# Optimization experiments

Measured on AMD Instinct MI355X. Metric: run time of the kernel, lower is better.

## Reference

```python
import jax, jax.numpy as jnp
import numpy as np

B, T, D = 4, 1024, 1024
H, KVH = 16, 4
HD = D // H
DFF = 4096
WINDOW = 256
EPS = 1e-5


def _layernorm(x, g, b):
    mu = jnp.mean(x, axis=-1, keepdims=True)
    var = jnp.mean(jnp.square(x - mu), axis=-1, keepdims=True)
    return (x - mu) * jax.lax.rsqrt(var + EPS) * g + b


def _rope(x):
    # x: (B, H, T, HD); non-interleaved halves, matching _apply_rope
    half = HD // 2
    theta = 1.0 / (10000.0 ** (jnp.arange(half, dtype=jnp.float32) / half))
    pos = jnp.arange(x.shape[2], dtype=jnp.float32)
    freqs = jnp.outer(pos, theta)            # (T, half)
    cos_f, sin_f = jnp.cos(freqs), jnp.sin(freqs)
    x1, x2 = x[..., :half], x[..., half:]
    return jnp.concatenate([x1 * cos_f - x2 * sin_f, x2 * cos_f + x1 * sin_f], axis=-1)


def setup_inputs() -> dict:
    key = jax.random.key(0)
    ks = jax.random.split(key, 16)
    s = 0.02
    d = {
        "x": jax.random.normal(ks[0], (B, T, D), dtype=jnp.float32),
        "Wq": jax.random.normal(ks[1], (D, H * HD), dtype=jnp.float32) * s,
        "bq": jnp.zeros((H * HD,), jnp.float32),
        "Wk": jax.random.normal(ks[2], (D, KVH * HD), dtype=jnp.float32) * s,
        "bk": jnp.zeros((KVH * HD,), jnp.float32),
        "Wv": jax.random.normal(ks[3], (D, KVH * HD), dtype=jnp.float32) * s,
        "bv": jnp.zeros((KVH * HD,), jnp.float32),
        "Wo": jax.random.normal(ks[4], (D, D), dtype=jnp.float32) * s,
        "bo": jnp.zeros((D,), jnp.float32),
        "g1": jnp.ones((D,), jnp.float32),
        "b1": jnp.zeros((D,), jnp.float32),
        "Wf1": jax.random.normal(ks[5], (D, DFF), dtype=jnp.float32) * s,
        "bf1": jnp.zeros((DFF,), jnp.float32),
        "Wf2": jax.random.normal(ks[6], (DFF, D), dtype=jnp.float32) * s,
        "bf2": jnp.zeros((D,), jnp.float32),
        "g2": jnp.ones((D,), jnp.float32),
        "b2": jnp.zeros((D,), jnp.float32),
    }
    return d


def reference(x, Wq, bq, Wk, bk, Wv, bv, Wo, bo, g1, b1, Wf1, bf1, Wf2, bf2, g2, b2):
    Bt, Tt, _ = x.shape
    h = _layernorm(x, g1, b1)
    q = (h @ Wq + bq).reshape(Bt, Tt, H, HD).transpose(0, 2, 1, 3)      # (B,H,T,HD)
    k = (h @ Wk + bk).reshape(Bt, Tt, KVH, HD).transpose(0, 2, 1, 3)    # (B,KVH,T,HD)
    v = (h @ Wv + bv).reshape(Bt, Tt, KVH, HD).transpose(0, 2, 1, 3)
    # GQA: repeat_interleave kv heads to nhead
    group = H // KVH
    k = jnp.repeat(k, group, axis=1)
    v = jnp.repeat(v, group, axis=1)
    q, k = _rope(q), _rope(k)
    scores = jnp.einsum("bhqd,bhkd->bhqk", q, k) / jnp.sqrt(jnp.float32(HD))
    # causal sliding-window mask: attend iff 0 <= (row-col) < WINDOW
    row = jnp.arange(Tt)[:, None]
    col = jnp.arange(Tt)[None, :]
    valid = (col <= row) & (row - col < WINDOW)
    scores = jnp.where(valid, scores, jnp.float32(-1e9))
    attn = jax.nn.softmax(scores, axis=-1)
    out = jnp.einsum("bhqk,bhkd->bhqd", attn, v)
    out = out.transpose(0, 2, 1, 3).reshape(Bt, Tt, D)
    x = x + (out @ Wo + bo)
    h2 = _layernorm(x, g2, b2)
    ff = jax.nn.gelu(h2 @ Wf1 + bf1, approximate=False) @ Wf2 + bf2
    return x + ff
```

## Files before the change

### kernel.cpp

```cpp
#include <hip/hip_runtime.h>
#include <hip/hip_bf16.h>
#include <math.h>

#define TT 1024
#define DD 1024
#define HH 16
#define KVHN 4
#define HDW 64
#define DFFN 4096
#define WIN 256

typedef __attribute__((ext_vector_type(4))) float f32x4;
typedef __attribute__((ext_vector_type(8))) __bf16 bf16x8;

typedef const __attribute__((address_space(1))) void gas_t;
typedef __attribute__((address_space(3))) void las_t;

__device__ inline unsigned short f2bf(float f){
  union { float f; unsigned u; } x; x.f = f;
  unsigned r = x.u + 0x7fffu + ((x.u >> 16) & 1u);
  return (unsigned short)(r >> 16);
}
__device__ inline float bf2f(unsigned short b){
  union { unsigned u; float f; } x; x.u = ((unsigned)b) << 16; return x.f;
}
__device__ inline f32x4 MFMA(bf16x8 a, bf16x8 b, f32x4 c){
  return __builtin_amdgcn_mfma_f32_16x16x32_bf16(a, b, c, 0, 0, 0);
}

__global__ void zero_k(float* out, int n){
  for (int i = blockIdx.x * blockDim.x + threadIdx.x; i < n; i += gridDim.x * blockDim.x)
    out[i] = 0.f;
}

__global__ __launch_bounds__(256) void wtrans_k(const float* __restrict__ W,
                                                unsigned short* __restrict__ Wt,
                                                int K, int N){
  __shared__ float t[32][33];
  int n0 = blockIdx.x * 32, k0 = blockIdx.y * 32;
  int tx = threadIdx.x & 31, ty = threadIdx.x >> 5;
#pragma unroll
  for (int i = 0; i < 4; i++){
    int kk = ty * 4 + i;
    t[kk][tx] = W[(size_t)(k0 + kk) * N + n0 + tx];
  }
  __syncthreads();
#pragma unroll
  for (int i = 0; i < 4; i++){
    int nn = ty * 4 + i;
    Wt[(size_t)(n0 + nn) * K + k0 + tx] = f2bf(t[tx][nn]);
  }
}

__global__ void packb_k(const float* bq, const float* bk, const float* bv, float* o){
  int i = blockIdx.x * 256 + threadIdx.x;
  if (i < 1536)
    o[i] = (i < 1024) ? bq[i] : ((i < 1280) ? bk[i - 1024] : bv[i - 1280]);
}

__global__ void finit_k(const float* __restrict__ x2, const float* __restrict__ bf2,
                        float* __restrict__ out){
  for (int i = blockIdx.x * blockDim.x + threadIdx.x; i < 4096 * 1024; i += gridDim.x * blockDim.x)
    out[i] = x2[i] + bf2[i & 1023];
}

__global__ __launch_bounds__(256) void ln_k(const float* __restrict__ x,
                                            const float* __restrict__ g,
                                            const float* __restrict__ b,
                                            unsigned short* __restrict__ out){
  __shared__ float red[4];
  int row = blockIdx.x, tid = threadIdx.x;
  const float* xr = x + (size_t)row * DD;
  float4 v = *(const float4*)(xr + tid * 4);
  float s = v.x + v.y + v.z + v.w;
#pragma unroll
  for (int off = 32; off; off >>= 1) s += __shfl_xor(s, off);
  if ((tid & 63) == 0) red[tid >> 6] = s;
  __syncthreads();
  float mu = (red[0] + red[1] + red[2] + red[3]) * (1.f / DD);
  __syncthreads();
  float dx = v.x - mu, dy = v.y - mu, dz = v.z - mu, dw = v.w - mu;
  float sq = dx*dx + dy*dy + dz*dz + dw*dw;
#pragma unroll
  for (int off = 32; off; off >>= 1) sq += __shfl_xor(sq, off);
  if ((tid & 63) == 0) red[tid >> 6] = sq;
  __syncthreads();
  float var = (red[0] + red[1] + red[2] + red[3]) * (1.f / DD);
  float inv = rsqrtf(var + 1e-5f);
  float4 gv = *(const float4*)(g + tid * 4);
  float4 bv = *(const float4*)(b + tid * 4);
  unsigned short* orow = out + (size_t)row * DD + tid * 4;
  orow[0] = f2bf(dx * inv * gv.x + bv.x);
  orow[1] = f2bf(dy * inv * gv.y + bv.y);
  orow[2] = f2bf(dz * inv * gv.z + bv.z);
  orow[3] = f2bf(dw * inv * gv.w + bv.w);
}

template<int EPI>
__global__ __launch_bounds__(512, 2) void gemm256_k(const unsigned short* __restrict__ A,
                                                    const unsigned short* __restrict__ Bt,
                                                    const float* __restrict__ bias,
                                                    void* __restrict__ Cout,
                                                    int M, int N, int Klen, int lda, int ldb){
  __shared__ unsigned short As2[2][16384];
  __shared__ unsigned short Bs2[2][16384];
  int tid = threadIdx.x;
  int row0 = blockIdx.x * 256, col0 = blockIdx.y * 256;
  int wid = tid >> 6, lane = tid & 63;
  int wr = wid >> 2, wc = wid & 3;
  int lr = lane & 15, lg = lane >> 4;
  int srow8 = tid >> 3;
  int schunk = (tid & 7) ^ (srow8 & 7);
  int xr8 = (lr & 7) << 3;
  f32x4 acc[8][4] = {};

  auto stageA = [&](int slot, int half, int ktn){
    const unsigned short* s0 = A + (size_t)(row0 + half*128 + srow8) * lda + ktn*64 + schunk*8;
    __builtin_amdgcn_global_load_lds((gas_t*)s0, (las_t*)&As2[slot][half*8192 + wid*512], 16, 0, 0);
    __builtin_amdgcn_global_load_lds((gas_t*)(s0 + (size_t)64*lda), (las_t*)&As2[slot][half*8192 + 4096 + wid*512], 16, 0, 0);
  };
  auto stageB = [&](int slot, int half, int ktn){
    const unsigned short* s0 = Bt + (size_t)(col0 + half*128 + srow8) * ldb + ktn*64 + schunk*8;
    __builtin_amdgcn_global_load_lds((gas_t*)s0, (las_t*)&Bs2[slot][half*8192 + wid*512], 16, 0, 0);
    __builtin_amdgcn_global_load_lds((gas_t*)(s0 + (size_t)64*ldb), (las_t*)&Bs2[slot][half*8192 + 4096 + wid*512], 16, 0, 0);
  };

  int NT = Klen >> 6;
  stageA(0, 0, 0); stageA(0, 1, 0); stageB(0, 0, 0); stageB(0, 1, 0);
  __syncthreads();

  for (int kt = 0; kt < NT; kt++){
    int s = kt & 1, ns = s ^ 1;
    bool pre = (kt + 1 < NT);
    const unsigned short* Ac = &As2[s][wr * 8192];
    const unsigned short* Bc = &Bs2[s][(wc >> 1) * 8192 + (wc & 1) * 4096];
    bf16x8 af[4][2], bf0[2][2], bf1[2][2];

#pragma unroll
    for (int mf = 0; mf < 4; mf++)
#pragma unroll
      for (int ks = 0; ks < 2; ks++)
        af[mf][ks] = *(const bf16x8*)&Ac[(mf*16 + lr)*64 + ((ks*32 + lg*8) ^ xr8)];
#pragma unroll
    for (int nf = 0; nf < 2; nf++)
#pragma unroll
      for (int ks = 0; ks < 2; ks++)
        bf0[nf][ks] = *(const bf16x8*)&Bc[(nf*16 + lr)*64 + ((ks*32 + lg*8) ^ xr8)];
    if (pre) stageA(ns, 0, kt + 1);
    __builtin_amdgcn_s_barrier();
    __builtin_amdgcn_s_setprio(1);
#pragma unroll
    for (int mf = 0; mf < 4; mf++)
#pragma unroll
      for (int nf = 0; nf < 2; nf++)
#pragma unroll
        for (int ks = 0; ks < 2; ks++)
          acc[mf][nf] = MFMA(af[mf][ks], bf0[nf][ks], acc[mf][nf]);
    __builtin_amdgcn_s_setprio(0);
    __builtin_amdgcn_s_barrier();

#pragma unroll
    for (int nf = 0; nf < 2; nf++)
#pragma unroll
      for (int ks = 0; ks < 2; ks++)
        bf1[nf][ks] = *(const bf16x8*)&Bc[((nf+2)*16 + lr)*64 + ((ks*32 + lg*8) ^ xr8)];
    if (pre) stageA(ns, 1, kt + 1);
    __builtin_amdgcn_s_barrier();
    __builtin_amdgcn_s_setprio(1);
#pragma unroll
    for (int mf = 0; mf < 4; mf++)
#pragma unroll
      for (int nf = 0; nf < 2; nf++)
#pragma unroll
        for (int ks = 0; ks < 2; ks++)
          acc[mf][nf+2] = MFMA(af[mf][ks], bf1[nf][ks], acc[mf][nf+2]);
    __builtin_amdgcn_s_setprio(0);
    __builtin_amdgcn_s_barrier();

#pragma unroll
    for (int mf = 0; mf < 4; mf++)
#pragma unroll
      for (int ks = 0; ks < 2; ks++)
        af[mf][ks] = *(const bf16x8*)&Ac[((mf+4)*16 + lr)*64 + ((ks*32 + lg*8) ^ xr8)];
    if (pre) stageB(ns, 0, kt + 1);
    __builtin_amdgcn_s_barrier();
    __builtin_amdgcn_s_setprio(1);
#pragma unroll
    for (int mf = 0; mf < 4; mf++)
#pragma unroll
      for (int nf = 0; nf < 2; nf++)
#pragma unroll
        for (int ks = 0; ks < 2; ks++)
          acc[mf+4][nf+2] = MFMA(af[mf][ks], bf1[nf][ks], acc[mf+4][nf+2]);
    __builtin_amdgcn_s_setprio(0);
    __builtin_amdgcn_s_barrier();

    if (pre) stageB(ns, 1, kt + 1);
    __builtin_amdgcn_s_barrier();
    __builtin_amdgcn_s_setprio(1);
#pragma unroll
    for (int mf = 0; mf < 4; mf++)
#pragma unroll
      for (int nf = 0; nf < 2; nf++)
#pragma unroll
        for (int ks = 0; ks < 2; ks++)
          acc[mf+4][nf] = MFMA(af[mf][ks], bf0[nf][ks], acc[mf+4][nf]);
    __builtin_amdgcn_s_setprio(0);
    __syncthreads();
  }

#pragma unroll
  for (int mf = 0; mf < 8; mf++){
#pragma unroll
    for (int r = 0; r < 4; r++){
      int gr = row0 + wr*128 + mf*16 + lg*4 + r;
#pragma unroll
      for (int nf = 0; nf < 4; nf++){
        int gc = col0 + wc*64 + nf*16 + lr;
        float val = acc[mf][nf][r] + bias[gc];
        if constexpr (EPI == 1){
          val = 0.5f * val * (1.f + erff(val * 0.70710678118f));
        }
        ((unsigned short*)Cout)[(size_t)gr * N + gc] = f2bf(val);
      }
    }
  }
}

template<int EPI>
__global__ __launch_bounds__(256) void gemm_k(const unsigned short* __restrict__ A,
                                              const unsigned short* __restrict__ Bt,
                                              const float* __restrict__ bias,
                                              const float* __restrict__ res,
                                              void* __restrict__ Cout,
                                              int M, int N, int Klen, int lda, int ldb){
  __shared__ unsigned short As[2][128 * 64];
  __shared__ unsigned short Bs[2][128 * 64];
  int tid = threadIdx.x;
  int row0 = blockIdx.x * 128, col0 = blockIdx.y * 128;
  A  += (size_t)blockIdx.z * Klen;
  Bt += (size_t)blockIdx.z * Klen;
  int wid = tid >> 6, lane = tid & 63;
  int wm = (wid >> 1) * 64, wn = (wid & 1) * 64;
  int lr = lane & 15, lg = lane >> 4;
  f32x4 acc[4][4] = {};

  int srow = wid * 8 + (lane >> 3);
  int scol = ((lane & 7) ^ (lane >> 3)) * 8;
  const unsigned short* gA0 = A  + (size_t)(row0 + srow) * lda + scol;
  const unsigned short* gB0 = Bt + (size_t)(col0 + srow) * ldb + scol;
  int lbase = wid * 512;

  int NT = Klen >> 6;
#pragma unroll
  for (int j = 0; j < 4; j++){
    __builtin_amdgcn_global_load_lds((gas_t*)(gA0 + (size_t)(j*32)*lda), (las_t*)&As[0][j*2048 + lbase], 16, 0, 0);
    __builtin_amdgcn_global_load_lds((gas_t*)(gB0 + (size_t)(j*32)*ldb), (las_t*)&Bs[0][j*2048 + lbase], 16, 0, 0);
  }
  __syncthreads();
  int cur = 0;
  int xr8 = (lr & 7) << 3;
  for (int t = 0; t < NT; t++){
    if (t + 1 < NT){
      int k0 = (t + 1) << 6;
      int nb = cur ^ 1;
#pragma unroll
      for (int j = 0; j < 4; j++){
        __builtin_amdgcn_global_load_lds((gas_t*)(gA0 + (size_t)(j*32)*lda + k0), (las_t*)&As[nb][j*2048 + lbase], 16, 0, 0);
        __builtin_amdgcn_global_load_lds((gas_t*)(gB0 + (size_t)(j*32)*ldb + k0), (las_t*)&Bs[nb][j*2048 + lbase], 16, 0, 0);
      }
    }
#pragma unroll
    for (int kk = 0; kk < 2; kk++){
      int xk = (kk*32 + lg*8) ^ xr8;
      bf16x8 af[4], bf[4];
#pragma unroll
      for (int mt = 0; mt < 4; mt++)
        af[mt] = *(const bf16x8*)&As[cur][(wm + mt*16 + lr) * 64 + xk];
#pragma unroll
      for (int nt2 = 0; nt2 < 4; nt2++)
        bf[nt2] = *(const bf16x8*)&Bs[cur][(wn + nt2*16 + lr) * 64 + xk];
#pragma unroll
      for (int mt = 0; mt < 4; mt++)
#pragma unroll
        for (int nt2 = 0; nt2 < 4; nt2++)
          acc[mt][nt2] = MFMA(af[mt], bf[nt2], acc[mt][nt2]);
    }
    __syncthreads();
    cur ^= 1;
  }
#pragma unroll
  for (int mt = 0; mt < 4; mt++){
#pragma unroll
    for (int r = 0; r < 4; r++){
      int gr = row0 + wm + mt*16 + lg*4 + r;
#pragma unroll
      for (int nt2 = 0; nt2 < 4; nt2++){
        int gc = col0 + wn + nt2*16 + lr;
        if constexpr (EPI == 5){
          unsafeAtomicAdd(&((float*)Cout)[(size_t)gr * N + gc], acc[mt][nt2][r]);
        } else {
          float val = acc[mt][nt2][r] + bias[gc];
          if constexpr (EPI == 1){
            val = 0.5f * val * (1.f + erff(val * 0.70710678118f));
          }
          if constexpr (EPI == 2){
            float ov = val + res[(size_t)gr * N + gc];
            ((float*)Cout)[(size_t)gr * N + gc] = ov;
          } else {
            ((unsigned short*)Cout)[(size_t)gr * N + gc] = f2bf(val);
          }
        }
      }
    }
  }
}

template<int NH>
__global__ __launch_bounds__(256) void rope_k(unsigned short* base, int rs){
  int idx = blockIdx.x * 8 + (threadIdx.x >> 5);
  int d = threadIdx.x & 31;
  int row = idx / NH;
  int head = idx % NH;
  int t = row & (TT - 1);
  unsigned short* p = base + (size_t)row * rs + head * HDW;
  float x1 = bf2f(p[d]);
  float x2 = bf2f(p[d + 32]);
  float theta = powf(10000.f, -(float)d * (1.f / 32.f));
  float c, s;
  sincosf((float)t * theta, &c, &s);
  p[d]      = f2bf(x1 * c + x2 * s);
  p[d + 32] = f2bf(x2 * c - x1 * s);
}

__global__ __launch_bounds__(256) void vtrans_k(const unsigned short* __restrict__ v, int rs,
                                                unsigned short* __restrict__ vt){
  __shared__ unsigned short tile[64][72];
  int t0 = blockIdx.x * 64;
  int kvh = blockIdx.y, b = blockIdx.z;
  int i = threadIdx.x;
  int tl = i >> 2, dc = (i & 3) * 16;
  const unsigned short* src = v + (size_t)(b * TT + t0 + tl) * rs + kvh * HDW + dc;
  *(uint4*)&tile[tl][dc]     = *(const uint4*)src;
  *(uint4*)&tile[tl][dc + 8] = *(const uint4*)(src + 8);
  __syncthreads();
  int d = i >> 2, tc = (i & 3) * 16;
  unsigned short tmp[16];
#pragma unroll
  for (int e = 0; e < 16; e++) tmp[e] = tile[tc + e][d];
  unsigned short* dst = vt + ((size_t)((b * KVHN + kvh) * HDW) + d) * TT + t0 + tc;
  *(uint4*)dst       = *(uint4*)tmp;
  *(uint4*)(dst + 8) = *(uint4*)(tmp + 8);
}

__global__ __launch_bounds__(64) void attn_k(const unsigned short* __restrict__ q, int qrs,
                                             const unsigned short* __restrict__ k, int krs,
                                             const unsigned short* __restrict__ vt,
                                             unsigned short* __restrict__ o){
  __shared__ unsigned short P[32 * 40];
  __shared__ float sc_l[32];
  int qt = blockIdx.x, h = blockIdx.y, b = blockIdx.z;
  int kvh = h >> 2;
  int lane = threadIdx.x;
  int lr = lane & 15, lg = lane >> 4;
  int q0 = qt * 32;
  bf16x8 qf[2][2];
#pragma unroll
  for (int qi = 0; qi < 2; qi++)
#pragma unroll
    for (int ks = 0; ks < 2; ks++)
      qf[qi][ks] = *(const bf16x8*)(q + (size_t)(b*TT + q0 + qi*16 + lr) * qrs + h * HDW + ks*32 + lg*8);
  f32x4 oa[2][4] = {};
  float m_st[2] = {-1e30f, -1e30f};
  float l_st[2] = {0.f, 0.f};
  int kt_lo = (q0 - (WIN - 1)) > 0 ? ((q0 - (WIN - 1)) >> 5) : 0;
  int kt_hi = (q0 + 31) >> 5;
  for (int kt = kt_lo; kt <= kt_hi; kt++){
    int kb = kt * 32;
    bf16x8 kf[2][2];
#pragma unroll
    for (int ki = 0; ki < 2; ki++)
#pragma unroll
      for (int ks = 0; ks < 2; ks++)
        kf[ki][ks] = *(const bf16x8*)(k + (size_t)(b*TT + kb + ki*16 + lr) * krs + kvh * HDW + ks*32 + lg*8);
    f32x4 s[2][2] = {};
#pragma unroll
    for (int ki = 0; ki < 2; ki++)
#pragma unroll
      for (int qi = 0; qi < 2; qi++){
        s[ki][qi] = MFMA(kf[ki][0], qf[qi][0], s[ki][qi]);
        s[ki][qi] = MFMA(kf[ki][1], qf[qi][1], s[ki][qi]);
      }
#pragma unroll
    for (int qi = 0; qi < 2; qi++){
      int qa = q0 + qi*16 + lr;
      float pv[8];
      float mx = -1e30f;
#pragma unroll
      for (int ki = 0; ki < 2; ki++)
#pragma unroll
        for (int r = 0; r < 4; r++){
          int ka = kb + ki*16 + lg*4 + r;
          float val = s[ki][qi][r] * 0.125f;
          bool ok = (ka <= qa) && (qa - ka < WIN);
          val = ok ? val : -1e9f;
          pv[ki*4 + r] = val;
          mx = fmaxf(mx, val);
        }
      mx = fmaxf(mx, __shfl_xor(mx, 16));
      mx = fmaxf(mx, __shfl_xor(mx, 32));
      float mn = fmaxf(m_st[qi], mx);
      float scl = __expf(m_st[qi] - mn);
      m_st[qi] = mn;
      float ls = 0.f;
#pragma unroll
      for (int j = 0; j < 8; j++){ float p = __expf(pv[j] - mn); pv[j] = p; ls += p; }
      ls += __shfl_xor(ls, 16);
      ls += __shfl_xor(ls, 32);
      l_st[qi] = l_st[qi] * scl + ls;
#pragma unroll
      for (int ki = 0; ki < 2; ki++){
        uint2 w;
        w.x = (unsigned)f2bf(pv[ki*4+0]) | ((unsigned)f2bf(pv[ki*4+1]) << 16);
        w.y = (unsigned)f2bf(pv[ki*4+2]) | ((unsigned)f2bf(pv[ki*4+3]) << 16);
        *(uint2*)&P[(qi*16 + lr) * 40 + ki*16 + lg*4] = w;
      }
      if (lg == 0) sc_l[qi*16 + lr] = scl;
    }
    __syncthreads();
#pragma unroll
    for (int qi = 0; qi < 2; qi++)
#pragma unroll
      for (int r = 0; r < 4; r++){
        float f = sc_l[qi*16 + lg*4 + r];
#pragma unroll
        for (int di = 0; di < 4; di++) oa[qi][di][r] *= f;
      }
    bf16x8 pa[2];
#pragma unroll
    for (int qi = 0; qi < 2; qi++)
      pa[qi] = *(const bf16x8*)&P[(qi*16 + lr) * 40 + lg*8];
#pragma unroll
    for (int di = 0; di < 4; di++){
      bf16x8 vb = *(const bf16x8*)(vt + ((size_t)((b*KVHN + kvh) * HDW) + di*16 + lr) * TT + kb + lg*8);
#pragma unroll
      for (int qi = 0; qi < 2; qi++)
        oa[qi][di] = MFMA(pa[qi], vb, oa[qi][di]);
    }
    __syncthreads();
  }
  if (lg == 0){ sc_l[lr] = l_st[0]; sc_l[16 + lr] = l_st[1]; }
  __syncthreads();
#pragma unroll
  for (int qi = 0; qi < 2; qi++)
#pragma unroll
    for (int r = 0; r < 4; r++){
      float inv = 1.f / sc_l[qi*16 + lg*4 + r];
      int t = q0 + qi*16 + lg*4 + r;
#pragma unroll
      for (int di = 0; di < 4; di++)
        o[((size_t)((b*TT + t) * HH) + h) * HDW + di*16 + lr] = f2bf(oa[qi][di][r] * inv);
    }
}

extern "C" void kernel_launch(void* const* d_in, const int* in_sizes, int n_in,
                              void* d_out, int out_size, void* d_ws, size_t ws_size,
                              hipStream_t stream){
  const float* x   = (const float*)d_in[0];
  const float* Wq  = (const float*)d_in[1];
  const float* bq  = (const float*)d_in[2];
  const float* Wk  = (const float*)d_in[3];
  const float* bk  = (const float*)d_in[4];
  const float* Wv  = (const float*)d_in[5];
  const float* bv  = (const float*)d_in[6];
  const float* Wo  = (const float*)d_in[7];
  const float* bo  = (const float*)d_in[8];
  const float* g1  = (const float*)d_in[9];
  const float* b1  = (const float*)d_in[10];
  const float* Wf1 = (const float*)d_in[11];
  const float* bf1 = (const float*)d_in[12];
  const float* Wf2 = (const float*)d_in[13];
  const float* bf2 = (const float*)d_in[14];
  const float* g2  = (const float*)d_in[15];
  const float* b2  = (const float*)d_in[16];

  static const int want[17] = {4194304, 1048576, 1024, 262144, 256, 262144, 256,
                               1048576, 1024, 1024, 1024, 4194304, 4096, 4194304,
                               1024, 1024, 1024};
  bool bad = (n_in != 17) || (out_size != 4194304);
  if (!bad) for (int i = 0; i < 17; i++) if (in_sizes[i] != want[i]) bad = true;
  if (bad){
    zero_k<<<2048, 256, 0, stream>>>((float*)d_out, out_size);
    return;
  }

  const int M = 4 * TT;
  const int QKVN = 1536;
  char* ws = (char*)d_ws;
  size_t off = 0;
  auto alloc = [&](size_t bytes) -> void* {
    void* p = ws + off; off += (bytes + 255) & ~(size_t)255; return p;
  };
  unsigned short* wqkv = (unsigned short*)alloc((size_t)QKVN * DD * 2);
  unsigned short* wto  = (unsigned short*)alloc((size_t)DD * DD * 2);
  unsigned short* wtf1 = (unsigned short*)alloc((size_t)DFFN * DD * 2);
  unsigned short* wtf2 = (unsigned short*)alloc((size_t)DD * DFFN * 2);
  float*          bqkv = (float*)alloc((size_t)QKVN * 4);
  unsigned short* h1   = (unsigned short*)alloc((size_t)M * DD * 2);
  unsigned short* qkv  = (unsigned short*)alloc((size_t)M * QKVN * 2);
  unsigned short* vtb  = (unsigned short*)alloc((size_t)M * 256 * 2);
  unsigned short* ao   = (unsigned short*)alloc((size_t)M * DD * 2);
  float*          x2   = (float*)alloc((size_t)M * DD * 4);
  unsigned short* h2   = h1;
  unsigned short* ff   = (unsigned short*)alloc((size_t)M * DFFN * 2);
  (void)ws_size;

  wtrans_k<<<dim3(DD/32,  DD/32),  256, 0, stream>>>(Wq,  wqkv,                       DD,  DD);
  wtrans_k<<<dim3(256/32, DD/32),  256, 0, stream>>>(Wk,  wqkv + (size_t)1024 * DD,   DD,  256);
  wtrans_k<<<dim3(256/32, DD/32),  256, 0, stream>>>(Wv,  wqkv + (size_t)1280 * DD,   DD,  256);
  wtrans_k<<<dim3(DD/32,  DD/32),  256, 0, stream>>>(Wo,  wto,  DD,  DD);
  wtrans_k<<<dim3(DFFN/32,DD/32),  256, 0, stream>>>(Wf1, wtf1, DD,  DFFN);
  wtrans_k<<<dim3(DD/32,  DFFN/32),256, 0, stream>>>(Wf2, wtf2, DFFN,DD);
  packb_k<<<6, 256, 0, stream>>>(bq, bk, bv, bqkv);

  ln_k<<<M, 256, 0, stream>>>(x, g1, b1, h1);

  gemm256_k<0><<<dim3(M/256, QKVN/256), 512, 0, stream>>>(h1, wqkv, bqkv, qkv, M, QKVN, DD, DD, DD);

  rope_k<HH>  <<<(M * HH) / 8,   256, 0, stream>>>(qkv,        QKVN);
  rope_k<KVHN><<<(M * KVHN) / 8, 256, 0, stream>>>(qkv + 1024, QKVN);

  vtrans_k<<<dim3(TT/64, KVHN, 4), 256, 0, stream>>>(qkv + 1280, QKVN, vtb);

  attn_k<<<dim3(TT/32, HH, 4), 64, 0, stream>>>(qkv, QKVN, qkv + 1024, QKVN, vtb, ao);

  gemm_k<2><<<dim3(M/128, DD/128), 256, 0, stream>>>(ao, wto, bo, x, x2, M, DD, DD, DD, DD);

  ln_k<<<M, 256, 0, stream>>>(x2, g2, b2, h2);

  gemm256_k<1><<<dim3(M/256, DFFN/256), 512, 0, stream>>>(h2, wtf1, bf1, ff, M, DFFN, DD, DD, DD);

  finit_k<<<2048, 256, 0, stream>>>(x2, bf2, (float*)d_out);
  gemm_k<5><<<dim3(M/128, DD/128, 2), 256, 0, stream>>>(ff, wtf2, nullptr, nullptr, (float*)d_out,
                                                        M, DD, 2048, DFFN, DFFN);
}
```

Measured before the change: 299.5 us.

## Restructure 256-tile GEMM prefetch with vmcnt waits and route QKV to 128-tile GEMM

The 256x256 GEMM kernel now issues the next K-tile's loads at the top of each iteration and waits with explicit s_waitcnt vmcnt counts. This replaces the four-phase barrier-interleaved staging and cuts the per-iteration barriers to two. Launch bounds drop to one block per CU. The QKV projection switches to the existing 128x128 gemm_k so that small GEMM gets more blocks. The risk is that the explicit vmcnt counting must match the number of outstanding loads, and the lower occupancy hint may change register allocation.

```diff
diff --git a/kernel.cpp b/kernel.cpp
--- a/kernel.cpp
+++ b/kernel.cpp
@@ -97,11 +97,11 @@
 }
 
 template<int EPI>
-__global__ __launch_bounds__(512, 2) void gemm256_k(const unsigned short* __restrict__ A,
-                                                    const unsigned short* __restrict__ Bt,
-                                                    const float* __restrict__ bias,
-                                                    void* __restrict__ Cout,
-                                                    int M, int N, int Klen, int lda, int ldb){
+__global__ __launch_bounds__(512, 1) void gemm256v_k(const unsigned short* __restrict__ A,
+                                                     const unsigned short* __restrict__ Bt,
+                                                     const float* __restrict__ bias,
+                                                     void* __restrict__ Cout,
+                                                     int M, int N, int Klen, int lda, int ldb){
   __shared__ unsigned short As2[2][16384];
   __shared__ unsigned short Bs2[2][16384];
   int tid = threadIdx.x;
@@ -126,12 +126,20 @@
   };
 
   int NT = Klen >> 6;
-  stageA(0, 0, 0); stageA(0, 1, 0); stageB(0, 0, 0); stageB(0, 1, 0);
-  __syncthreads();
+  stageA(0, 0, 0); stageB(0, 0, 0); stageA(0, 1, 0); stageB(0, 1, 0);
 
   for (int kt = 0; kt < NT; kt++){
     int s = kt & 1, ns = s ^ 1;
     bool pre = (kt + 1 < NT);
+    if (pre){
+      stageA(ns, 0, kt + 1); stageB(ns, 0, kt + 1);
+      asm volatile("s_waitcnt vmcnt(4)" ::: "memory");
+    } else {
+      asm volatile("s_waitcnt vmcnt(0)" ::: "memory");
+    }
+    __builtin_amdgcn_sched_barrier(0);
+    __builtin_amdgcn_s_barrier();
+
     const unsigned short* Ac = &As2[s][wr * 8192];
     const unsigned short* Bc = &Bs2[s][(wc >> 1) * 8192 + (wc & 1) * 4096];
     bf16x8 af[4][2], bf0[2][2], bf1[2][2];
@@ -146,8 +154,6 @@
 #pragma unroll
       for (int ks = 0; ks < 2; ks++)
         bf0[nf][ks] = *(const bf16x8*)&Bc[(nf*16 + lr)*64 + ((ks*32 + lg*8) ^ xr8)];
-    if (pre) stageA(ns, 0, kt + 1);
-    __builtin_amdgcn_s_barrier();
     __builtin_amdgcn_s_setprio(1);
 #pragma unroll
     for (int mf = 0; mf < 4; mf++)
@@ -157,15 +163,13 @@
         for (int ks = 0; ks < 2; ks++)
           acc[mf][nf] = MFMA(af[mf][ks], bf0[nf][ks], acc[mf][nf]);
     __builtin_amdgcn_s_setprio(0);
-    __builtin_amdgcn_s_barrier();
+    if (pre){ stageA(ns, 1, kt + 1); stageB(ns, 1, kt + 1); }
 
 #pragma unroll
     for (int nf = 0; nf < 2; nf++)
 #pragma unroll
       for (int ks = 0; ks < 2; ks++)
         bf1[nf][ks] = *(const bf16x8*)&Bc[((nf+2)*16 + lr)*64 + ((ks*32 + lg*8) ^ xr8)];
-    if (pre) stageA(ns, 1, kt + 1);
-    __builtin_amdgcn_s_barrier();
     __builtin_amdgcn_s_setprio(1);
 #pragma unroll
     for (int mf = 0; mf < 4; mf++)
@@ -175,15 +179,12 @@
         for (int ks = 0; ks < 2; ks++)
           acc[mf][nf+2] = MFMA(af[mf][ks], bf1[nf][ks], acc[mf][nf+2]);
     __builtin_amdgcn_s_setprio(0);
-    __builtin_amdgcn_s_barrier();
 
 #pragma unroll
     for (int mf = 0; mf < 4; mf++)
 #pragma unroll
       for (int ks = 0; ks < 2; ks++)
         af[mf][ks] = *(const bf16x8*)&Ac[((mf+4)*16 + lr)*64 + ((ks*32 + lg*8) ^ xr8)];
-    if (pre) stageB(ns, 0, kt + 1);
-    __builtin_amdgcn_s_barrier();
     __builtin_amdgcn_s_setprio(1);
 #pragma unroll
     for (int mf = 0; mf < 4; mf++)
@@ -192,12 +193,7 @@
 #pragma unroll
         for (int ks = 0; ks < 2; ks++)
           acc[mf+4][nf+2] = MFMA(af[mf][ks], bf1[nf][ks], acc[mf+4][nf+2]);
-    __builtin_amdgcn_s_setprio(0);
-    __builtin_amdgcn_s_barrier();
-
-    if (pre) stageB(ns, 1, kt + 1);
-    __builtin_amdgcn_s_barrier();
-    __builtin_amdgcn_s_setprio(1);
+
 #pragma unroll
     for (int mf = 0; mf < 4; mf++)
 #pragma unroll
@@ -206,7 +202,8 @@
         for (int ks = 0; ks < 2; ks++)
           acc[mf+4][nf] = MFMA(af[mf][ks], bf0[nf][ks], acc[mf+4][nf]);
     __builtin_amdgcn_s_setprio(0);
-    __syncthreads();
+    __builtin_amdgcn_sched_barrier(0);
+    __builtin_amdgcn_s_barrier();
   }
 
 #pragma unroll
@@ -525,7 +522,7 @@
 
   ln_k<<<M, 256, 0, stream>>>(x, g1, b1, h1);
 
-  gemm256_k<0><<<dim3(M/256, QKVN/256), 512, 0, stream>>>(h1, wqkv, bqkv, qkv, M, QKVN, DD, DD, DD);
+  gemm_k<0><<<dim3(M/128, QKVN/128), 256, 0, stream>>>(h1, wqkv, bqkv, nullptr, qkv, M, QKVN, DD, DD, DD);
 
   rope_k<HH>  <<<(M * HH) / 8,   256, 0, stream>>>(qkv,        QKVN);
   rope_k<KVHN><<<(M * KVHN) / 8, 256, 0, stream>>>(qkv + 1024, QKVN);
@@ -538,7 +535,7 @@
 
   ln_k<<<M, 256, 0, stream>>>(x2, g2, b2, h2);
 
-  gemm256_k<1><<<dim3(M/256, DFFN/256), 512, 0, stream>>>(h2, wtf1, bf1, ff, M, DFFN, DD, DD, DD);
+  gemm256v_k<1><<<dim3(M/256, DFFN/256), 512, 0, stream>>>(h2, wtf1, bf1, ff, M, DFFN, DD, DD, DD);
 
   finit_k<<<2048, 256, 0, stream>>>(x2, bf2, (float*)d_out);
   gemm_k<5><<<dim3(M/128, DD/128, 2), 256, 0, stream>>>(ff, wtf2, nullptr, nullptr, (float*)d_out,
```

Result: no change. 298.9 us (-0.2%).
